# Kernel optimization log

Measured on AMD Instinct MI355X. Metric: run time of the kernel, lower is better.

Reference implementation:

```python
import jax, jax.numpy as jnp
import numpy as np

B, S = 32, 2048
D = 128      # embedding_dim
H = 256      # hidden_dim
K = 512      # codebook_size
RECON_COEF, COMMIT_COEF, VQ_COEF = 1.0, 0.15, 0.05


def _conv1d(x, w, b):
    # x: [B, Cin, S], w: [Cout, Cin, 3], 'SAME' padding (padding=1, k=3)
    y = jax.lax.conv_general_dilated(x, w, window_strides=(1,), padding='SAME',
                                     dimension_numbers=('NCH', 'OIH', 'NCH'))
    return y + b[None, :, None]


def _lrelu(x):
    return jnp.where(x >= 0, x, 0.2 * x)


def setup_inputs() -> dict:
    key = jax.random.key(0)
    ks = jax.random.split(key, 14)

    def w(k, shape, fan_in):
        bound = 1.0 / np.sqrt(fan_in)
        return jax.random.uniform(k, shape, jnp.float32, -bound, bound)

    return {
        'x': jax.random.normal(ks[0], (B, S), jnp.float32),
        'codebook': jax.random.normal(ks[1], (K, D), jnp.float32),
        'ew1': w(ks[2], (H, 1, 3), 1 * 3),  'eb1': w(ks[3], (H,), 1 * 3),
        'ew2': w(ks[4], (H, H, 3), H * 3),  'eb2': w(ks[5], (H,), H * 3),
        'ew3': w(ks[6], (D, H, 3), H * 3),  'eb3': w(ks[7], (D,), H * 3),
        'dw1': w(ks[8], (H, D, 3), D * 3),  'db1': w(ks[9], (H,), D * 3),
        'dw2': w(ks[10], (H, H, 3), H * 3), 'db2': w(ks[11], (H,), H * 3),
        'dw3': w(ks[12], (1, H, 3), H * 3), 'db3': w(ks[13], (1,), H * 3),
    }


def reference(x, codebook, ew1, eb1, ew2, eb2, ew3, eb3, dw1, db1, dw2, db2, dw3, db3):
    # ---- encode ----
    h = x[:, None, :]                                  # [B,1,S]
    h = _lrelu(_conv1d(h, ew1, eb1))
    h = _lrelu(_conv1d(h, ew2, eb2))
    z = _conv1d(h, ew3, eb3)                           # [B,D,S]

    # ---- vector quantize (eval mode: no EMA update) ----
    zt = jnp.transpose(z, (0, 2, 1))                   # [B,S,D]
    z_flat = zt.reshape(-1, D)                         # [B*S,D]
    # squared distances: |z|^2 + |c|^2 - 2 z c^T
    d = (jnp.sum(z_flat ** 2, axis=1, keepdims=True)
         + jnp.sum(codebook ** 2, axis=1)
         - 2.0 * z_flat @ codebook.T)                  # [B*S,K]
    idx = jnp.argmin(d, axis=1)                        # [B*S]
    z_q = codebook[idx].reshape(zt.shape)              # [B,S,D] (== one-hot @ codebook)

    vq_loss = jnp.mean((jax.lax.stop_gradient(zt) - z_q) ** 2) * VQ_COEF
    commitment_loss = jnp.mean((zt - jax.lax.stop_gradient(z_q)) ** 2) * COMMIT_COEF
    indices = idx.reshape(B, S)

    # ---- decode ----
    h = jnp.transpose(z_q, (0, 2, 1))                  # [B,D,S]
    h = _lrelu(_conv1d(h, dw1, db1))
    h = _lrelu(_conv1d(h, dw2, db2))
    x_recon = _conv1d(h, dw3, db3)[:, 0, :]            # [B,S]

    recon_loss = jnp.mean((x - x_recon) ** 2) * RECON_COEF
    loss = recon_loss + vq_loss + commitment_loss
    return x_recon, indices, loss, recon_loss, vq_loss, commitment_loss
```

## Files before the change

kernel.cpp:

```cpp
#include <hip/hip_runtime.h>
#include <float.h>

#define S_LEN 2048
#define BATCH 32
#define HCH   256
#define DCH   128
#define KCODES 512

typedef float  f32x4  __attribute__((ext_vector_type(4)));
typedef short  bf16x8 __attribute__((ext_vector_type(8)));
typedef short  short8 __attribute__((ext_vector_type(8)));

__device__ __forceinline__ float lrelu_f(float v) { return v >= 0.f ? v : 0.2f * v; }

__device__ __forceinline__ short f2bf(float f) {
    unsigned u = __float_as_uint(f);
    u = u + 0x7fffu + ((u >> 16) & 1u);
    return (short)(u >> 16);
}
__device__ __forceinline__ float bf2f(unsigned short u) {
    return __uint_as_float(((unsigned)u) << 16);
}

__device__ __forceinline__ void async_copy16(short* lds, const short* g) {
    __builtin_amdgcn_global_load_lds(
        (const __attribute__((address_space(1))) unsigned int*)g,
        (__attribute__((address_space(3))) unsigned int*)lds,
        16, 0, 0);
}

__global__ void prep_cb_split_kernel(const float* __restrict__ cb,
                                     short* __restrict__ cb_hi, short* __restrict__ cb_lo,
                                     float* __restrict__ cnorm) {
    int k = blockIdx.x * 256 + threadIdx.x;
    if (k < KCODES) {
        float s = 0.f;
        for (int d = 0; d < DCH; ++d) {
            float v = cb[k * DCH + d];
            s += v * v;
            short hi = f2bf(v);
            short lo = f2bf(v - bf2f((unsigned short)hi));
            cb_hi[k * DCH + d] = hi;
            cb_lo[k * DCH + d] = lo;
        }
        cnorm[k] = s;
    }
}

__global__ void prep_w_split_kernel(const float* __restrict__ Wsrc,
                                    short* __restrict__ Wh, short* __restrict__ Wl,
                                    int Cout, int Cin) {
    int i = blockIdx.x * 256 + threadIdx.x;
    int total = 3 * Cout * Cin;
    if (i < total) {
        int t = i / (Cout * Cin);
        int rem = i - t * Cout * Cin;
        int co = rem / Cin;
        int ci = rem - co * Cin;
        float v = Wsrc[(co * Cin + ci) * 3 + t];
        short hi = f2bf(v);
        Wh[i] = hi;
        Wl[i] = f2bf(v - bf2f((unsigned short)hi));
    }
}

__global__ void prep_wdec_kernel(const float* __restrict__ Wsrc, short* __restrict__ Wdst,
                                 int Cin) {
    int i = blockIdx.x * 256 + threadIdx.x;
    int total = 3 * 256 * Cin;
    if (i < total) {
        int t = i / (256 * Cin);
        int rem = i - t * 256 * Cin;
        int co = rem / Cin;
        int ci = rem - co * Cin;
        Wdst[i] = f2bf(Wsrc[(co * Cin + ci) * 3 + t]);
    }
}

__global__ void prep_w3t_kernel(const float* __restrict__ w3, float* __restrict__ w3t) {
    int i = blockIdx.x * 256 + threadIdx.x;
    if (i < 768) {
        int t = i / 256, ci = i - t * 256;
        w3t[i] = w3[ci * 3 + t];
    }
}

__global__ __launch_bounds__(256) void enc_conv1_cl_kernel(
        const float* __restrict__ x, short* __restrict__ h_hi, short* __restrict__ h_lo,
        const float* __restrict__ w, const float* __restrict__ bias) {
    __shared__ float ws[HCH * 3];
    __shared__ float bs[HCH];
    int tid = threadIdx.x;
    for (int i = tid; i < HCH * 3; i += 256) ws[i] = w[i];
    for (int i = tid; i < HCH; i += 256) bs[i] = bias[i];
    __syncthreads();
    int b = blockIdx.y;
    int s = blockIdx.x * 32 + (tid >> 3);
    int cch = tid & 7;
    const float* xb = x + (size_t)b * S_LEN;
    float xm = (s > 0) ? xb[s - 1] : 0.f;
    float x0 = xb[s];
    float xp = (s < S_LEN - 1) ? xb[s + 1] : 0.f;
    size_t base = ((size_t)(b * S_LEN + s)) * HCH + cch * 32;
#pragma unroll
    for (int cc = 0; cc < 4; ++cc) {
        short8 oh, ol;
#pragma unroll
        for (int e = 0; e < 8; ++e) {
            int co = cch * 32 + cc * 8 + e;
            float v = ws[co * 3 + 0] * xm + ws[co * 3 + 1] * x0 + ws[co * 3 + 2] * xp + bs[co];
            v = lrelu_f(v);
            short hi = f2bf(v);
            oh[e] = hi;
            ol[e] = f2bf(v - bf2f((unsigned short)hi));
        }
        *(short8*)(h_hi + base + cc * 8) = oh;
        *(short8*)(h_lo + base + cc * 8) = ol;
    }
}

__global__ __launch_bounds__(256, 3) void conv_mfma_split(
        const short* __restrict__ in_hi, const short* __restrict__ in_lo,
        short* __restrict__ out_hi, short* __restrict__ out_lo,
        const short* __restrict__ wt_hi, const short* __restrict__ wt_lo,
        const float* __restrict__ bias, int Cin, int Cout, int do_lrelu) {
    __shared__ short smem[16640];

    const int tid  = threadIdx.x;
    const int lane = tid & 63;
    const int w    = tid >> 6;
    const int m    = lane & 15;
    const int q    = lane >> 4;
    const int sOff = (w & 1) * 64;
    const int cOff = (w >> 1) * 64;
    const int b    = blockIdx.z;
    const int s0   = blockIdx.x * 128;
    const int co0  = blockIdx.y * 128;

    f32x4 acc[4][4];
    f32x4 zero4 = {0.f, 0.f, 0.f, 0.f};
#pragma unroll
    for (int i = 0; i < 4; ++i)
#pragma unroll
        for (int j = 0; j < 4; ++j) acc[i][j] = zero4;

    const short* inhb = in_hi + (size_t)b * S_LEN * Cin;
    const short* inlb = in_lo + (size_t)b * S_LEN * Cin;
    const char* XhB = (const char*)smem;
    const char* XlB = XhB + 1040 * 16;

    for (int ci0 = 0; ci0 < Cin; ci0 += 64) {
        __syncthreads();

        if (s0 == 0 && tid < 16) {
            short8 z = {0, 0, 0, 0, 0, 0, 0, 0};
            int buf = tid >> 3, slot = tid & 7;
            *(short8*)(smem + (size_t)(buf * 1040 + slot) * 8) = z;
        }
        if (s0 == S_LEN - 128 && tid < 16) {
            short8 z = {0, 0, 0, 0, 0, 0, 0, 0};
            int buf = tid >> 3, slot = tid & 7;
            *(short8*)(smem + (size_t)(buf * 1040 + 129 * 8 + slot) * 8) = z;
        }

        for (int c = tid; c < 2080; c += 256) {
            int base_c = c - lane;
            int buf  = (c >= 1040) ? 1 : 0;
            int cc   = c - buf * 1040;
            int r    = cc >> 3;
            int slot = cc & 7;
            int gch  = slot ^ (r & 7);
            int s    = s0 - 1 + r;
            short* ldsb = smem + (size_t)base_c * 8;
            const short* gp = (buf ? inlb : inhb) + (size_t)s * Cin + ci0 + gch * 8;
            if (s >= 0 && s < S_LEN) async_copy16(ldsb, gp);
        }
        __syncthreads();

#pragma unroll 1
        for (int ks = 0; ks < 2; ++ks) {
#pragma unroll
            for (int t = 0; t < 3; ++t) {
                bf16x8 ah[4], al[4], bh[4], bl[4];
#pragma unroll
                for (int i = 0; i < 4; ++i) {
                    int row = sOff + i * 16 + m + t;
                    int off = row * 128 + (((ks * 4 + q) ^ (row & 7)) << 4);
                    ah[i] = *(const bf16x8*)(XhB + off);
                    al[i] = *(const bf16x8*)(XlB + off);
                }
#pragma unroll
                for (int j = 0; j < 4; ++j) {
                    size_t woff = ((size_t)(t * Cout + co0 + cOff + j * 16 + m)) * Cin
                                  + ci0 + ks * 32 + q * 8;
                    bh[j] = *(const bf16x8*)(wt_hi + woff);
                    bl[j] = *(const bf16x8*)(wt_lo + woff);
                }
#pragma unroll
                for (int i = 0; i < 4; ++i)
#pragma unroll
                    for (int j = 0; j < 4; ++j) {
                        acc[i][j] = __builtin_amdgcn_mfma_f32_16x16x32_bf16(ah[i], bh[j], acc[i][j], 0, 0, 0);
                        acc[i][j] = __builtin_amdgcn_mfma_f32_16x16x32_bf16(ah[i], bl[j], acc[i][j], 0, 0, 0);
                        acc[i][j] = __builtin_amdgcn_mfma_f32_16x16x32_bf16(al[i], bh[j], acc[i][j], 0, 0, 0);
                    }
            }
        }
    }

    __syncthreads();

    short* ob = smem + w * 4096;
#pragma unroll
    for (int pass = 0; pass < 2; ++pass) {
#pragma unroll
        for (int j = 0; j < 4; ++j) {
            float bv = bias[co0 + cOff + j * 16 + m];
#pragma unroll
            for (int i = 0; i < 4; ++i)
#pragma unroll
                for (int r = 0; r < 4; ++r) {
                    float val = acc[i][j][r] + bv;
                    if (do_lrelu) val = lrelu_f(val);
                    short hi = f2bf(val);
                    short v = pass ? f2bf(val - bf2f((unsigned short)hi)) : hi;
                    ob[(i * 16 + q * 4 + r) * 64 + j * 16 + m] = v;
                }
        }
        short* outp = pass ? out_lo : out_hi;
#pragma unroll
        for (int itr = 0; itr < 8; ++itr) {
            int row = itr * 8 + (lane >> 3);
            int ch  = lane & 7;
            short8 v = *(const short8*)(ob + row * 64 + ch * 8);
            size_t goff = ((size_t)(b * S_LEN + s0 + sOff + row)) * Cout
                          + co0 + cOff + ch * 8;
            *(short8*)(outp + goff) = v;
        }
    }
}

__global__ __launch_bounds__(256) void vq_mfma_kernel(
        const short* __restrict__ z_hi, const short* __restrict__ z_lo,
        const short* __restrict__ cb_hi, const short* __restrict__ cb_lo,
        const float* __restrict__ cnorm, const float* __restrict__ cb,
        int* __restrict__ idx_out, float* __restrict__ idx_f_out,
        short* __restrict__ zq, float* __restrict__ acc_vq) {
    __shared__ short smem[2 * 64 * 136];
    __shared__ float redv[64][4];
    __shared__ int   redi[64][4];
    __shared__ int   idxs[64];
    __shared__ float wsum2[4];
    short* Zh = smem;
    short* Zl = smem + 64 * 136;

    const int tid = threadIdx.x;
    const int lane = tid & 63;
    const int w = tid >> 6;
    const int m = lane & 15;
    const int q = lane >> 4;
    const int n0 = blockIdx.x * 64;

    for (int c = tid; c < 2048; c += 256) {
        int buf = c >> 10;
        int rem = c & 1023;
        int r = rem >> 4, part = rem & 15;
        size_t goff = (size_t)(n0 + r) * DCH + part * 8;
        float4 v = buf ? *(const float4*)(z_lo + goff) : *(const float4*)(z_hi + goff);
        *(float4*)((buf ? Zl : Zh) + r * 136 + part * 8) = v;
    }
    __syncthreads();

    float best[4][4];
    int besti[4][4];
#pragma unroll
    for (int i = 0; i < 4; ++i)
#pragma unroll
        for (int r = 0; r < 4; ++r) { best[i][r] = FLT_MAX; besti[i][r] = 0; }

    for (int k0 = 0; k0 < KCODES; k0 += 256) {
        f32x4 acc[4][4];
        f32x4 zero4 = {0.f, 0.f, 0.f, 0.f};
#pragma unroll
        for (int i = 0; i < 4; ++i)
#pragma unroll
            for (int j = 0; j < 4; ++j) acc[i][j] = zero4;

#pragma unroll
        for (int d0 = 0; d0 < DCH; d0 += 32) {
            bf16x8 ah[4], al[4], bh[4], bl[4];
#pragma unroll
            for (int i = 0; i < 4; ++i) {
                int row = i * 16 + m;
                ah[i] = *(const bf16x8*)(Zh + row * 136 + d0 + q * 8);
                al[i] = *(const bf16x8*)(Zl + row * 136 + d0 + q * 8);
            }
#pragma unroll
            for (int j = 0; j < 4; ++j) {
                size_t coff = (size_t)(k0 + w * 64 + j * 16 + m) * DCH + d0 + q * 8;
                bh[j] = *(const bf16x8*)(cb_hi + coff);
                bl[j] = *(const bf16x8*)(cb_lo + coff);
            }
#pragma unroll
            for (int i = 0; i < 4; ++i)
#pragma unroll
                for (int j = 0; j < 4; ++j) {
                    acc[i][j] = __builtin_amdgcn_mfma_f32_16x16x32_bf16(ah[i], bh[j], acc[i][j], 0, 0, 0);
                    acc[i][j] = __builtin_amdgcn_mfma_f32_16x16x32_bf16(ah[i], bl[j], acc[i][j], 0, 0, 0);
                    acc[i][j] = __builtin_amdgcn_mfma_f32_16x16x32_bf16(al[i], bh[j], acc[i][j], 0, 0, 0);
                }
        }
#pragma unroll
        for (int j = 0; j < 4; ++j) {
            int k = k0 + w * 64 + j * 16 + m;
            float cn = cnorm[k];
#pragma unroll
            for (int i = 0; i < 4; ++i)
#pragma unroll
                for (int r = 0; r < 4; ++r) {
                    float dv = cn - 2.f * acc[i][j][r];
                    if (dv < best[i][r]) { best[i][r] = dv; besti[i][r] = k; }
                }
        }
    }

#pragma unroll
    for (int mask = 1; mask < 16; mask <<= 1) {
#pragma unroll
        for (int i = 0; i < 4; ++i)
#pragma unroll
            for (int r = 0; r < 4; ++r) {
                float ov = __shfl_xor(best[i][r], mask);
                int oi = __shfl_xor(besti[i][r], mask);
                if (ov < best[i][r] || (ov == best[i][r] && oi < besti[i][r])) {
                    best[i][r] = ov; besti[i][r] = oi;
                }
            }
    }
    if (m == 0) {
#pragma unroll
        for (int i = 0; i < 4; ++i)
#pragma unroll
            for (int r = 0; r < 4; ++r) {
                int srow = i * 16 + q * 4 + r;
                redv[srow][w] = best[i][r];
                redi[srow][w] = besti[i][r];
            }
    }
    __syncthreads();
    if (tid < 64) {
        float bv = redv[tid][0];
        int bi = redi[tid][0];
#pragma unroll
        for (int w2 = 1; w2 < 4; ++w2) {
            float v = redv[tid][w2];
            int ii = redi[tid][w2];
            if (v < bv || (v == bv && ii < bi)) { bv = v; bi = ii; }
        }
        int n = n0 + tid;
        idx_out[n] = bi;
        idx_f_out[n] = (float)bi;
        idxs[tid] = bi;
    }
    __syncthreads();

    {
        int r = tid >> 2;
        int dpart = tid & 3;
        int k = idxs[r];
        const float* src = cb + (size_t)k * DCH + dpart * 32;
        const short* zh = Zh + r * 136 + dpart * 32;
        const short* zl = Zl + r * 136 + dpart * 32;
        size_t zoff = (size_t)(n0 + r) * DCH + dpart * 32;
        float sum = 0.f;
#pragma unroll
        for (int h = 0; h < 4; ++h) {
            float4 f0 = *(const float4*)(src + h * 8);
            float4 f1 = *(const float4*)(src + h * 8 + 4);
            bf16x8 vh = *(const bf16x8*)(zh + h * 8);
            bf16x8 vl = *(const bf16x8*)(zl + h * 8);
            float qv[8] = {f0.x, f0.y, f0.z, f0.w, f1.x, f1.y, f1.z, f1.w};
            short8 o;
#pragma unroll
            for (int e = 0; e < 8; ++e) {
                o[e] = f2bf(qv[e]);
                float zv = bf2f((unsigned short)vh[e]) + bf2f((unsigned short)vl[e]);
                float df = zv - qv[e];
                sum += df * df;
            }
            *(short8*)(zq + zoff + h * 8) = o;
        }
        for (int off = 32; off > 0; off >>= 1) sum += __shfl_down(sum, off);
        if (lane == 0) wsum2[w] = sum;
    }
    __syncthreads();
    if (tid == 0) atomicAdd(acc_vq, wsum2[0] + wsum2[1] + wsum2[2] + wsum2[3]);
}

__global__ __launch_bounds__(256) void conv_mfma_cl(
        const short* __restrict__ in, short* __restrict__ out,
        const short* __restrict__ wt, const float* __restrict__ bias,
        int Cin) {
    __shared__ short smem[24672];
    short* Xs = smem;
    short* Ws = smem + 130 * 48;

    const int tid = threadIdx.x;
    const int lane = tid & 63;
    const int w = tid >> 6;
    const int m = lane & 15;
    const int q = lane >> 4;
    const int sOff = (w & 1) * 64;
    const int cOff = (w >> 1) * 64;
    const int b = blockIdx.z;
    const int s0 = blockIdx.x * 128;
    const int co0 = blockIdx.y * 128;

    f32x4 acc[4][4];
    f32x4 zero4 = {0.f, 0.f, 0.f, 0.f};
#pragma unroll
    for (int i = 0; i < 4; ++i)
#pragma unroll
        for (int j = 0; j < 4; ++j) acc[i][j] = zero4;

    const short* inb = in + (size_t)b * S_LEN * Cin;

    for (int ci0 = 0; ci0 < Cin; ci0 += 32) {
        __syncthreads();
        for (int c = tid; c < 520; c += 256) {
            int r = c >> 2, part = c & 3;
            int s = s0 - 1 + r;
            float4 v = make_float4(0.f, 0.f, 0.f, 0.f);
            if (s >= 0 && s < S_LEN)
                v = *(const float4*)(inb + (size_t)s * Cin + ci0 + part * 8);
            *(float4*)(Xs + r * 48 + part * 8) = v;
        }
        for (int c = tid; c < 1536; c += 256) {
            int t = c >> 9;
            int rem = c & 511;
            int cr = rem >> 2, part = rem & 3;
            float4 v = *(const float4*)(wt + ((size_t)(t * 256 + co0 + cr)) * Cin + ci0 + part * 8);
            *(float4*)(Ws + (t * 128 + cr) * 48 + part * 8) = v;
        }
        __syncthreads();

#pragma unroll
        for (int t = 0; t < 3; ++t) {
            bf16x8 a[4], bb[4];
#pragma unroll
            for (int i = 0; i < 4; ++i)
                a[i] = *(const bf16x8*)(Xs + (sOff + i * 16 + m + t) * 48 + q * 8);
#pragma unroll
            for (int j = 0; j < 4; ++j)
                bb[j] = *(const bf16x8*)(Ws + (t * 128 + cOff + j * 16 + m) * 48 + q * 8);
#pragma unroll
            for (int i = 0; i < 4; ++i)
#pragma unroll
                for (int j = 0; j < 4; ++j)
                    acc[i][j] = __builtin_amdgcn_mfma_f32_16x16x32_bf16(
                        a[i], bb[j], acc[i][j], 0, 0, 0);
        }
    }

    __syncthreads();

    short* ob = smem + w * (64 * 80);
#pragma unroll
    for (int j = 0; j < 4; ++j) {
        float bv = bias[co0 + cOff + j * 16 + m];
#pragma unroll
        for (int i = 0; i < 4; ++i) {
#pragma unroll
            for (int r = 0; r < 4; ++r) {
                float val = acc[i][j][r] + bv;
                val = lrelu_f(val);
                ob[(i * 16 + q * 4 + r) * 80 + j * 16 + m] = f2bf(val);
            }
        }
    }
    const int rsel = lane >> 3;
    const int off8 = (lane & 7) * 8;
#pragma unroll
    for (int pass = 0; pass < 8; ++pass) {
        int rr = pass * 8 + rsel;
        short8 v = *(const short8*)(ob + rr * 80 + off8);
        *(short8*)(out + ((size_t)(b * S_LEN + s0 + sOff + rr)) * 256 + co0 + cOff + off8) = v;
    }
}

__global__ __launch_bounds__(256) void dec_conv3_tiled_kernel(
        const short* __restrict__ h, const float* __restrict__ w3t,
        const float* __restrict__ b3, const float* __restrict__ x,
        float* __restrict__ xr, float* __restrict__ acc_recon) {
    __shared__ short Zs[66 * 264];
    __shared__ float ws[3 * 256];
    __shared__ float wsum[4];
    int tid = threadIdx.x;
    int b = blockIdx.y;
    int s0 = blockIdx.x * 64;
    const short* hb = h + (size_t)b * S_LEN * HCH;
    for (int i = tid; i < 768; i += 256) ws[i] = w3t[i];
    for (int c = tid; c < 2112; c += 256) {
        int r = c >> 5, part = c & 31;
        int g = s0 - 1 + r;
        short8 v = {0, 0, 0, 0, 0, 0, 0, 0};
        if (g >= 0 && g < S_LEN)
            v = *(const short8*)(hb + (size_t)g * HCH + part * 8);
        *(short8*)(Zs + r * 264 + part * 8) = v;
    }
    __syncthreads();

    int quarter = tid & 3;
    int sl = tid >> 2;
    float a0 = 0.f, a1 = 0.f, a2 = 0.f, a3 = 0.f;
#pragma unroll
    for (int t = 0; t < 3; ++t) {
        const short* zrow = Zs + (sl + t) * 264 + quarter * 64;
        const float* wrow = ws + t * 256 + quarter * 64;
#pragma unroll
        for (int c = 0; c < 8; ++c) {
            bf16x8 v = *(const bf16x8*)(zrow + c * 8);
            float4 w0 = *(const float4*)(wrow + c * 8);
            float4 w1 = *(const float4*)(wrow + c * 8 + 4);
            a0 = fmaf(w0.x, bf2f((unsigned short)v[0]), a0);
            a1 = fmaf(w0.y, bf2f((unsigned short)v[1]), a1);
            a2 = fmaf(w0.z, bf2f((unsigned short)v[2]), a2);
            a3 = fmaf(w0.w, bf2f((unsigned short)v[3]), a3);
            a0 = fmaf(w1.x, bf2f((unsigned short)v[4]), a0);
            a1 = fmaf(w1.y, bf2f((unsigned short)v[5]), a1);
            a2 = fmaf(w1.z, bf2f((unsigned short)v[6]), a2);
            a3 = fmaf(w1.w, bf2f((unsigned short)v[7]), a3);
        }
    }
    float acc = (a0 + a1) + (a2 + a3);
    acc += __shfl_xor(acc, 1);
    acc += __shfl_xor(acc, 2);
    float df2 = 0.f;
    if (quarter == 0) {
        int s = s0 + sl;
        float tot = acc + b3[0];
        xr[b * S_LEN + s] = tot;
        float df = x[b * S_LEN + s] - tot;
        df2 = df * df;
    }
    for (int off = 32; off > 0; off >>= 1) df2 += __shfl_down(df2, off);
    int lane = tid & 63, wv = tid >> 6;
    if (lane == 0) wsum[wv] = df2;
    __syncthreads();
    if (tid == 0) atomicAdd(acc_recon, wsum[0] + wsum[1] + wsum[2] + wsum[3]);
}

__global__ void finalize_kernel(const float* __restrict__ accs, float* __restrict__ out) {
    if (threadIdx.x == 0) {
        float vqm = accs[0] / ((float)BATCH * S_LEN * DCH);
        float rm  = accs[1] / ((float)BATCH * S_LEN);
        float vq_loss = vqm * 0.05f;
        float commit  = vqm * 0.15f;
        float recon   = rm * 1.0f;
        out[0] = recon + vq_loss + commit;
        out[1] = recon;
        out[2] = vq_loss;
        out[3] = commit;
    }
}

extern "C" void kernel_launch(void* const* d_in, const int* in_sizes, int n_in,
                              void* d_out, int out_size, void* d_ws, size_t ws_size,
                              hipStream_t stream) {
    const float* x    = (const float*)d_in[0];
    const float* cb   = (const float*)d_in[1];
    const float* ew1  = (const float*)d_in[2];
    const float* eb1  = (const float*)d_in[3];
    const float* ew2  = (const float*)d_in[4];
    const float* eb2  = (const float*)d_in[5];
    const float* ew3  = (const float*)d_in[6];
    const float* eb3  = (const float*)d_in[7];
    const float* dw1  = (const float*)d_in[8];
    const float* db1  = (const float*)d_in[9];
    const float* dw2  = (const float*)d_in[10];
    const float* db2  = (const float*)d_in[11];
    const float* dw3  = (const float*)d_in[12];
    const float* db3  = (const float*)d_in[13];

    float* out = (float*)d_out;
    float* xr    = out;
    float* idx_f = out + BATCH * S_LEN;
    float* loss_out = out + 2 * BATCH * S_LEN;

    const size_t NH = (size_t)BATCH * S_LEN * HCH;
    const size_t ND = (size_t)BATCH * S_LEN * DCH;

    short* sp = (short*)d_ws;
    short* h1_hi = sp;
    short* h1_lo = sp + NH;
    short* z_hi  = sp;
    short* z_lo  = sp + ND;
    short* h1d_bf = sp;
    short* h2_hi = sp + 2 * NH;
    short* h2_lo = sp + 3 * NH;
    short* zq_bf = sp + 2 * NH;
    short* h2d_bf = sp + 3 * NH;
    short* sm = sp + 4 * NH;
    short* cb_hi = sm; sm += KCODES * DCH;
    short* cb_lo = sm; sm += KCODES * DCH;
    short* w2_hi = sm; sm += 3 * HCH * HCH;
    short* w2_lo = sm; sm += 3 * HCH * HCH;
    short* w3_hi = sm; sm += 3 * DCH * HCH;
    short* w3_lo = sm; sm += 3 * DCH * HCH;
    short* wbf_d1 = sm; sm += 3 * 256 * DCH;
    short* wbf_d2 = sm; sm += 3 * 256 * HCH;
    float* cnorm = (float*)sm;
    int* idxb = (int*)(cnorm + KCODES);
    float* w3t = (float*)(idxb + BATCH * S_LEN);
    float* accs = w3t + 768;

    hipMemsetAsync(accs, 0, 2 * sizeof(float), stream);

    prep_cb_split_kernel<<<2, 256, 0, stream>>>(cb, cb_hi, cb_lo, cnorm);
    prep_w_split_kernel<<<(3 * HCH * HCH + 255) / 256, 256, 0, stream>>>(ew2, w2_hi, w2_lo, HCH, HCH);
    prep_w_split_kernel<<<(3 * DCH * HCH + 255) / 256, 256, 0, stream>>>(ew3, w3_hi, w3_lo, DCH, HCH);
    prep_wdec_kernel<<<(3 * 256 * DCH + 255) / 256, 256, 0, stream>>>(dw1, wbf_d1, DCH);
    prep_wdec_kernel<<<(3 * 256 * HCH + 255) / 256, 256, 0, stream>>>(dw2, wbf_d2, HCH);
    prep_w3t_kernel<<<3, 256, 0, stream>>>(dw3, w3t);

    enc_conv1_cl_kernel<<<dim3(S_LEN / 32, BATCH), 256, 0, stream>>>(x, h1_hi, h1_lo, ew1, eb1);
    conv_mfma_split<<<dim3(S_LEN / 128, HCH / 128, BATCH), 256, 0, stream>>>(
        h1_hi, h1_lo, h2_hi, h2_lo, w2_hi, w2_lo, eb2, HCH, HCH, 1);
    conv_mfma_split<<<dim3(S_LEN / 128, DCH / 128, BATCH), 256, 0, stream>>>(
        h2_hi, h2_lo, z_hi, z_lo, w3_hi, w3_lo, eb3, HCH, DCH, 0);

    vq_mfma_kernel<<<(BATCH * S_LEN) / 64, 256, 0, stream>>>(
        z_hi, z_lo, cb_hi, cb_lo, cnorm, cb, idxb, idx_f, zq_bf, accs);

    conv_mfma_cl<<<dim3(S_LEN / 128, 2, BATCH), 256, 0, stream>>>(
        zq_bf, h1d_bf, wbf_d1, db1, DCH);
    conv_mfma_cl<<<dim3(S_LEN / 128, 2, BATCH), 256, 0, stream>>>(
        h1d_bf, h2d_bf, wbf_d2, db2, HCH);
    dec_conv3_tiled_kernel<<<dim3(S_LEN / 64, BATCH), 256, 0, stream>>>(
        h2d_bf, w3t, db3, x, xr, accs + 1);

    finalize_kernel<<<1, 64, 0, stream>>>(accs, loss_out);
}
```

Before: 492.4 us.

## Restructure conv MFMA kernel with swizzled async LDS input and direct-global weights

The channels-last conv kernel now stages only the input tile in LDS, using async 16-byte copies into an XOR-swizzled layout to avoid bank conflicts. Weight fragments are read straight from global memory (relying on cache) rather than being staged in LDS. The input-channel step grows from 32 to 64, and launch bounds request 3 blocks per CU, which the smaller LDS footprint makes possible. The aim is fewer LDS stores and barriers and higher occupancy. The cost is more global/L2 traffic for weights and possible latency stalls before the MFMAs.

Measured after the change: 506.1 us. +2.8%, slower.

```diff
diff --git a/kernel.cpp b/kernel.cpp
--- a/kernel.cpp
+++ b/kernel.cpp
@@ -397,24 +397,22 @@
     if (tid == 0) atomicAdd(acc_vq, wsum2[0] + wsum2[1] + wsum2[2] + wsum2[3]);
 }
 
-__global__ __launch_bounds__(256) void conv_mfma_cl(
+__global__ __launch_bounds__(256, 3) void conv_mfma_cl(
         const short* __restrict__ in, short* __restrict__ out,
         const short* __restrict__ wt, const float* __restrict__ bias,
         int Cin) {
-    __shared__ short smem[24672];
-    short* Xs = smem;
-    short* Ws = smem + 130 * 48;
-
-    const int tid = threadIdx.x;
+    __shared__ short smem[16384];
+
+    const int tid  = threadIdx.x;
     const int lane = tid & 63;
-    const int w = tid >> 6;
-    const int m = lane & 15;
-    const int q = lane >> 4;
+    const int w    = tid >> 6;
+    const int m    = lane & 15;
+    const int q    = lane >> 4;
     const int sOff = (w & 1) * 64;
     const int cOff = (w >> 1) * 64;
-    const int b = blockIdx.z;
-    const int s0 = blockIdx.x * 128;
-    const int co0 = blockIdx.y * 128;
+    const int b    = blockIdx.z;
+    const int s0   = blockIdx.x * 128;
+    const int co0  = blockIdx.y * 128;
 
     f32x4 acc[4][4];
     f32x4 zero4 = {0.f, 0.f, 0.f, 0.f};
@@ -424,67 +422,82 @@
         for (int j = 0; j < 4; ++j) acc[i][j] = zero4;
 
     const short* inb = in + (size_t)b * S_LEN * Cin;
-
-    for (int ci0 = 0; ci0 < Cin; ci0 += 32) {
+    const char* XB = (const char*)smem;
+
+    for (int ci0 = 0; ci0 < Cin; ci0 += 64) {
         __syncthreads();
-        for (int c = tid; c < 520; c += 256) {
-            int r = c >> 2, part = c & 3;
-            int s = s0 - 1 + r;
-            float4 v = make_float4(0.f, 0.f, 0.f, 0.f);
-            if (s >= 0 && s < S_LEN)
-                v = *(const float4*)(inb + (size_t)s * Cin + ci0 + part * 8);
-            *(float4*)(Xs + r * 48 + part * 8) = v;
-        }
-        for (int c = tid; c < 1536; c += 256) {
-            int t = c >> 9;
-            int rem = c & 511;
-            int cr = rem >> 2, part = rem & 3;
-            float4 v = *(const float4*)(wt + ((size_t)(t * 256 + co0 + cr)) * Cin + ci0 + part * 8);
-            *(float4*)(Ws + (t * 128 + cr) * 48 + part * 8) = v;
+
+        if (s0 == 0 && tid < 8) {
+            short8 z = {0, 0, 0, 0, 0, 0, 0, 0};
+            *(short8*)(smem + (size_t)tid * 8) = z;
+        }
+        if (s0 == S_LEN - 128 && tid < 8) {
+            short8 z = {0, 0, 0, 0, 0, 0, 0, 0};
+            *(short8*)(smem + (size_t)(129 * 8 + tid) * 8) = z;
+        }
+
+        for (int c = tid; c < 1040; c += 256) {
+            int base_c = c - lane;
+            int r    = c >> 3;
+            int slot = c & 7;
+            int gch  = slot ^ (r & 7);
+            int s    = s0 - 1 + r;
+            short* ldsb = smem + (size_t)base_c * 8;
+            const short* gp = inb + (size_t)s * Cin + ci0 + gch * 8;
+            if (s >= 0 && s < S_LEN) async_copy16(ldsb, gp);
         }
         __syncthreads();
 
-#pragma unroll
-        for (int t = 0; t < 3; ++t) {
-            bf16x8 a[4], bb[4];
-#pragma unroll
-            for (int i = 0; i < 4; ++i)
-                a[i] = *(const bf16x8*)(Xs + (sOff + i * 16 + m + t) * 48 + q * 8);
-#pragma unroll
-            for (int j = 0; j < 4; ++j)
-                bb[j] = *(const bf16x8*)(Ws + (t * 128 + cOff + j * 16 + m) * 48 + q * 8);
-#pragma unroll
-            for (int i = 0; i < 4; ++i)
-#pragma unroll
-                for (int j = 0; j < 4; ++j)
-                    acc[i][j] = __builtin_amdgcn_mfma_f32_16x16x32_bf16(
-                        a[i], bb[j], acc[i][j], 0, 0, 0);
-        }
-    }
-
-    __syncthreads();
-
-    short* ob = smem + w * (64 * 80);
+#pragma unroll 1
+        for (int ks = 0; ks < 2; ++ks) {
+#pragma unroll
+            for (int t = 0; t < 3; ++t) {
+                bf16x8 a[4], bb[4];
+#pragma unroll
+                for (int i = 0; i < 4; ++i) {
+                    int row = sOff + i * 16 + m + t;
+                    int off = row * 128 + (((ks * 4 + q) ^ (row & 7)) << 4);
+                    a[i] = *(const bf16x8*)(XB + off);
+                }
+#pragma unroll
+                for (int j = 0; j < 4; ++j) {
+                    size_t woff = ((size_t)(t * 256 + co0 + cOff + j * 16 + m)) * Cin
+                                  + ci0 + ks * 32 + q * 8;
+                    bb[j] = *(const bf16x8*)(wt + woff);
+                }
+#pragma unroll
+                for (int i = 0; i < 4; ++i)
+#pragma unroll
+                    for (int j = 0; j < 4; ++j)
+                        acc[i][j] = __builtin_amdgcn_mfma_f32_16x16x32_bf16(
+                            a[i], bb[j], acc[i][j], 0, 0, 0);
+            }
+        }
+    }
+
+    __syncthreads();
+
+    short* ob = smem + w * 4096;
 #pragma unroll
     for (int j = 0; j < 4; ++j) {
         float bv = bias[co0 + cOff + j * 16 + m];
 #pragma unroll
-        for (int i = 0; i < 4; ++i) {
+        for (int i = 0; i < 4; ++i)
 #pragma unroll
             for (int r = 0; r < 4; ++r) {
                 float val = acc[i][j][r] + bv;
                 val = lrelu_f(val);
-                ob[(i * 16 + q * 4 + r) * 80 + j * 16 + m] = f2bf(val);
-            }
-        }
-    }
-    const int rsel = lane >> 3;
-    const int off8 = (lane & 7) * 8;
-#pragma unroll
-    for (int pass = 0; pass < 8; ++pass) {
-        int rr = pass * 8 + rsel;
-        short8 v = *(const short8*)(ob + rr * 80 + off8);
-        *(short8*)(out + ((size_t)(b * S_LEN + s0 + sOff + rr)) * 256 + co0 + cOff + off8) = v;
+                ob[(i * 16 + q * 4 + r) * 64 + j * 16 + m] = f2bf(val);
+            }
+    }
+#pragma unroll
+    for (int itr = 0; itr < 8; ++itr) {
+        int row = itr * 8 + (lane >> 3);
+        int ch  = lane & 7;
+        short8 v = *(const short8*)(ob + row * 64 + ch * 8);
+        size_t goff = ((size_t)(b * S_LEN + s0 + sOff + row)) * 256
+                      + co0 + cOff + ch * 8;
+        *(short8*)(out + goff) = v;
     }
 }
 
```

## Fuse final encoder conv with vector quantization and merge prep kernels

Applied to the files above, without the earlier changes.

The last encoder convolution now runs in the same kernel as the codebook search. Its hi/lo bf16 output goes straight into shared memory, so z no longer makes a round trip through global memory and one launch is dropped. The six weight and codebook preparation kernels are merged into one launch with a job index on the grid's y dimension. The cost is a larger, serialized fused kernel with launch bounds targeting two blocks per CU. The int index buffer is also removed.

Result: no change. 492.5 us (+0.0%).

```diff
diff --git a/kernel.cpp b/kernel.cpp
--- a/kernel.cpp
+++ b/kernel.cpp
@@ -29,59 +29,62 @@
         16, 0, 0);
 }
 
-__global__ void prep_cb_split_kernel(const float* __restrict__ cb,
-                                     short* __restrict__ cb_hi, short* __restrict__ cb_lo,
-                                     float* __restrict__ cnorm) {
-    int k = blockIdx.x * 256 + threadIdx.x;
-    if (k < KCODES) {
-        float s = 0.f;
-        for (int d = 0; d < DCH; ++d) {
-            float v = cb[k * DCH + d];
-            s += v * v;
+__global__ void prep_all_kernel(
+        const float* __restrict__ cb, short* __restrict__ cb_hi,
+        short* __restrict__ cb_lo, float* __restrict__ cnorm,
+        const float* __restrict__ ew2, short* __restrict__ w2_hi, short* __restrict__ w2_lo,
+        const float* __restrict__ ew3, short* __restrict__ w3_hi, short* __restrict__ w3_lo,
+        const float* __restrict__ dw1, short* __restrict__ wbf_d1,
+        const float* __restrict__ dw2, short* __restrict__ wbf_d2,
+        const float* __restrict__ dw3, float* __restrict__ w3t) {
+    const int job = blockIdx.y;
+    const int i = blockIdx.x * 256 + threadIdx.x;
+    if (job == 0) {
+        if (i < KCODES) {
+            float s = 0.f;
+            for (int d = 0; d < DCH; ++d) {
+                float v = cb[i * DCH + d];
+                s += v * v;
+                short hi = f2bf(v);
+                cb_hi[i * DCH + d] = hi;
+                cb_lo[i * DCH + d] = f2bf(v - bf2f((unsigned short)hi));
+            }
+            cnorm[i] = s;
+        }
+    } else if (job == 1 || job == 2) {
+        const int Cout = (job == 1) ? 256 : 128;
+        const int Cin = 256;
+        const float* src = (job == 1) ? ew2 : ew3;
+        short* Wh = (job == 1) ? w2_hi : w3_hi;
+        short* Wl = (job == 1) ? w2_lo : w3_lo;
+        int total = 3 * Cout * Cin;
+        if (i < total) {
+            int t = i / (Cout * Cin);
+            int rem = i - t * Cout * Cin;
+            int co = rem / Cin;
+            int ci = rem - co * Cin;
+            float v = src[(co * Cin + ci) * 3 + t];
             short hi = f2bf(v);
-            short lo = f2bf(v - bf2f((unsigned short)hi));
-            cb_hi[k * DCH + d] = hi;
-            cb_lo[k * DCH + d] = lo;
-        }
-        cnorm[k] = s;
-    }
-}
-
-__global__ void prep_w_split_kernel(const float* __restrict__ Wsrc,
-                                    short* __restrict__ Wh, short* __restrict__ Wl,
-                                    int Cout, int Cin) {
-    int i = blockIdx.x * 256 + threadIdx.x;
-    int total = 3 * Cout * Cin;
-    if (i < total) {
-        int t = i / (Cout * Cin);
-        int rem = i - t * Cout * Cin;
-        int co = rem / Cin;
-        int ci = rem - co * Cin;
-        float v = Wsrc[(co * Cin + ci) * 3 + t];
-        short hi = f2bf(v);
-        Wh[i] = hi;
-        Wl[i] = f2bf(v - bf2f((unsigned short)hi));
-    }
-}
-
-__global__ void prep_wdec_kernel(const float* __restrict__ Wsrc, short* __restrict__ Wdst,
-                                 int Cin) {
-    int i = blockIdx.x * 256 + threadIdx.x;
-    int total = 3 * 256 * Cin;
-    if (i < total) {
-        int t = i / (256 * Cin);
-        int rem = i - t * 256 * Cin;
-        int co = rem / Cin;
-        int ci = rem - co * Cin;
-        Wdst[i] = f2bf(Wsrc[(co * Cin + ci) * 3 + t]);
-    }
-}
-
-__global__ void prep_w3t_kernel(const float* __restrict__ w3, float* __restrict__ w3t) {
-    int i = blockIdx.x * 256 + threadIdx.x;
-    if (i < 768) {
-        int t = i / 256, ci = i - t * 256;
-        w3t[i] = w3[ci * 3 + t];
+            Wh[i] = hi;
+            Wl[i] = f2bf(v - bf2f((unsigned short)hi));
+        }
+    } else if (job == 3 || job == 4) {
+        const int Cin = (job == 3) ? 128 : 256;
+        const float* src = (job == 3) ? dw1 : dw2;
+        short* Wd = (job == 3) ? wbf_d1 : wbf_d2;
+        int total = 3 * 256 * Cin;
+        if (i < total) {
+            int t = i / (256 * Cin);
+            int rem = i - t * 256 * Cin;
+            int co = rem / Cin;
+            int ci = rem - co * Cin;
+            Wd[i] = f2bf(src[(co * Cin + ci) * 3 + t]);
+        }
+    } else {
+        if (i < 768) {
+            int t = i / 256, ci = i - t * 256;
+            w3t[i] = dw3[ci * 3 + t];
+        }
     }
 }
 
@@ -240,161 +243,253 @@
     }
 }
 
-__global__ __launch_bounds__(256) void vq_mfma_kernel(
-        const short* __restrict__ z_hi, const short* __restrict__ z_lo,
+__global__ __launch_bounds__(256, 2) void conv3_vq_kernel(
+        const short* __restrict__ in_hi, const short* __restrict__ in_lo,
+        const short* __restrict__ wt_hi, const short* __restrict__ wt_lo,
+        const float* __restrict__ bias,
         const short* __restrict__ cb_hi, const short* __restrict__ cb_lo,
         const float* __restrict__ cnorm, const float* __restrict__ cb,
-        int* __restrict__ idx_out, float* __restrict__ idx_f_out,
-        short* __restrict__ zq, float* __restrict__ acc_vq) {
-    __shared__ short smem[2 * 64 * 136];
+        float* __restrict__ idx_f_out, short* __restrict__ zq,
+        float* __restrict__ acc_vq) {
+    __shared__ short smem[17408];
     __shared__ float redv[64][4];
     __shared__ int   redi[64][4];
     __shared__ int   idxs[64];
     __shared__ float wsum2[4];
+
+    const int tid  = threadIdx.x;
+    const int lane = tid & 63;
+    const int w    = tid >> 6;
+    const int m    = lane & 15;
+    const int q    = lane >> 4;
+    const int sOff = (w & 1) * 64;
+    const int cOff = (w >> 1) * 64;
+    const int b    = blockIdx.y;
+    const int s0   = blockIdx.x * 128;
+    const int Cin  = HCH;
+
+    f32x4 acc[4][4];
+    f32x4 zero4 = {0.f, 0.f, 0.f, 0.f};
+#pragma unroll
+    for (int i = 0; i < 4; ++i)
+#pragma unroll
+        for (int j = 0; j < 4; ++j) acc[i][j] = zero4;
+
+    const short* inhb = in_hi + (size_t)b * S_LEN * Cin;
+    const short* inlb = in_lo + (size_t)b * S_LEN * Cin;
+    const char* XhB = (const char*)smem;
+    const char* XlB = XhB + 1040 * 16;
+
+    for (int ci0 = 0; ci0 < Cin; ci0 += 64) {
+        __syncthreads();
+
+        if (s0 == 0 && tid < 16) {
+            short8 z = {0, 0, 0, 0, 0, 0, 0, 0};
+            int buf = tid >> 3, slot = tid & 7;
+            *(short8*)(smem + (size_t)(buf * 1040 + slot) * 8) = z;
+        }
+        if (s0 == S_LEN - 128 && tid < 16) {
+            short8 z = {0, 0, 0, 0, 0, 0, 0, 0};
+            int buf = tid >> 3, slot = tid & 7;
+            *(short8*)(smem + (size_t)(buf * 1040 + 129 * 8 + slot) * 8) = z;
+        }
+
+        for (int c = tid; c < 2080; c += 256) {
+            int base_c = c - lane;
+            int buf  = (c >= 1040) ? 1 : 0;
+            int cc   = c - buf * 1040;
+            int r    = cc >> 3;
+            int slot = cc & 7;
+            int gch  = slot ^ (r & 7);
+            int s    = s0 - 1 + r;
+            short* ldsb = smem + (size_t)base_c * 8;
+            const short* gp = (buf ? inlb : inhb) + (size_t)s * Cin + ci0 + gch * 8;
+            if (s >= 0 && s < S_LEN) async_copy16(ldsb, gp);
+        }
+        __syncthreads();
+
+#pragma unroll 1
+        for (int ks = 0; ks < 2; ++ks) {
+#pragma unroll
+            for (int t = 0; t < 3; ++t) {
+                bf16x8 ah[4], al[4], bh[4], bl[4];
+#pragma unroll
+                for (int i = 0; i < 4; ++i) {
+                    int row = sOff + i * 16 + m + t;
+                    int off = row * 128 + (((ks * 4 + q) ^ (row & 7)) << 4);
+                    ah[i] = *(const bf16x8*)(XhB + off);
+                    al[i] = *(const bf16x8*)(XlB + off);
+                }
+#pragma unroll
+                for (int j = 0; j < 4; ++j) {
+                    size_t woff = ((size_t)(t * DCH + cOff + j * 16 + m)) * Cin
+                                  + ci0 + ks * 32 + q * 8;
+                    bh[j] = *(const bf16x8*)(wt_hi + woff);
+                    bl[j] = *(const bf16x8*)(wt_lo + woff);
+                }
+#pragma unroll
+                for (int i = 0; i < 4; ++i)
+#pragma unroll
+                    for (int j = 0; j < 4; ++j) {
+                        acc[i][j] = __builtin_amdgcn_mfma_f32_16x16x32_bf16(ah[i], bh[j], acc[i][j], 0, 0, 0);
+                        acc[i][j] = __builtin_amdgcn_mfma_f32_16x16x32_bf16(ah[i], bl[j], acc[i][j], 0, 0, 0);
+                        acc[i][j] = __builtin_amdgcn_mfma_f32_16x16x32_bf16(al[i], bh[j], acc[i][j], 0, 0, 0);
+                    }
+            }
+        }
+    }
+
+    __syncthreads();
+
     short* Zh = smem;
-    short* Zl = smem + 64 * 136;
-
-    const int tid = threadIdx.x;
-    const int lane = tid & 63;
-    const int w = tid >> 6;
-    const int m = lane & 15;
-    const int q = lane >> 4;
-    const int n0 = blockIdx.x * 64;
-
-    for (int c = tid; c < 2048; c += 256) {
-        int buf = c >> 10;
-        int rem = c & 1023;
-        int r = rem >> 4, part = rem & 15;
-        size_t goff = (size_t)(n0 + r) * DCH + part * 8;
-        float4 v = buf ? *(const float4*)(z_lo + goff) : *(const float4*)(z_hi + goff);
-        *(float4*)((buf ? Zl : Zh) + r * 136 + part * 8) = v;
-    }
-    __syncthreads();
-
-    float best[4][4];
-    int besti[4][4];
-#pragma unroll
-    for (int i = 0; i < 4; ++i)
-#pragma unroll
-        for (int r = 0; r < 4; ++r) { best[i][r] = FLT_MAX; besti[i][r] = 0; }
-
-    for (int k0 = 0; k0 < KCODES; k0 += 256) {
-        f32x4 acc[4][4];
-        f32x4 zero4 = {0.f, 0.f, 0.f, 0.f};
+    short* Zl = smem + 8704;
+
+#pragma unroll 1
+    for (int pass = 0; pass < 2; ++pass) {
+        if ((w & 1) == pass) {
+#pragma unroll
+            for (int j = 0; j < 4; ++j) {
+                float bv = bias[cOff + j * 16 + m];
+#pragma unroll
+                for (int i = 0; i < 4; ++i)
+#pragma unroll
+                    for (int r = 0; r < 4; ++r) {
+                        float val = acc[i][j][r] + bv;
+                        short hi = f2bf(val);
+                        short lo = f2bf(val - bf2f((unsigned short)hi));
+                        int rc = (i * 16 + q * 4 + r) * 136 + cOff + j * 16 + m;
+                        Zh[rc] = hi;
+                        Zl[rc] = lo;
+                    }
+            }
+        }
+        __syncthreads();
+
+        const int n0 = b * S_LEN + s0 + pass * 64;
+
+        float best[4][4];
+        int besti[4][4];
 #pragma unroll
         for (int i = 0; i < 4; ++i)
 #pragma unroll
-            for (int j = 0; j < 4; ++j) acc[i][j] = zero4;
-
-#pragma unroll
-        for (int d0 = 0; d0 < DCH; d0 += 32) {
-            bf16x8 ah[4], al[4], bh[4], bl[4];
-#pragma unroll
-            for (int i = 0; i < 4; ++i) {
-                int row = i * 16 + m;
-                ah[i] = *(const bf16x8*)(Zh + row * 136 + d0 + q * 8);
-                al[i] = *(const bf16x8*)(Zl + row * 136 + d0 + q * 8);
+            for (int r = 0; r < 4; ++r) { best[i][r] = FLT_MAX; besti[i][r] = 0; }
+
+#pragma unroll 1
+        for (int k0 = 0; k0 < KCODES; k0 += 256) {
+            f32x4 vacc[4][4];
+#pragma unroll
+            for (int i = 0; i < 4; ++i)
+#pragma unroll
+                for (int j = 0; j < 4; ++j) vacc[i][j] = zero4;
+
+#pragma unroll
+            for (int d0 = 0; d0 < DCH; d0 += 32) {
+                bf16x8 ah[4], al[4], bh[4], bl[4];
+#pragma unroll
+                for (int i = 0; i < 4; ++i) {
+                    int row = i * 16 + m;
+                    ah[i] = *(const bf16x8*)(Zh + row * 136 + d0 + q * 8);
+                    al[i] = *(const bf16x8*)(Zl + row * 136 + d0 + q * 8);
+                }
+#pragma unroll
+                for (int j = 0; j < 4; ++j) {
+                    size_t coff = (size_t)(k0 + w * 64 + j * 16 + m) * DCH + d0 + q * 8;
+                    bh[j] = *(const bf16x8*)(cb_hi + coff);
+                    bl[j] = *(const bf16x8*)(cb_lo + coff);
+                }
+#pragma unroll
+                for (int i = 0; i < 4; ++i)
+#pragma unroll
+                    for (int j = 0; j < 4; ++j) {
+                        vacc[i][j] = __builtin_amdgcn_mfma_f32_16x16x32_bf16(ah[i], bh[j], vacc[i][j], 0, 0, 0);
+                        vacc[i][j] = __builtin_amdgcn_mfma_f32_16x16x32_bf16(ah[i], bl[j], vacc[i][j], 0, 0, 0);
+                        vacc[i][j] = __builtin_amdgcn_mfma_f32_16x16x32_bf16(al[i], bh[j], vacc[i][j], 0, 0, 0);
+                    }
             }
 #pragma unroll
             for (int j = 0; j < 4; ++j) {
-                size_t coff = (size_t)(k0 + w * 64 + j * 16 + m) * DCH + d0 + q * 8;
-                bh[j] = *(const bf16x8*)(cb_hi + coff);
-                bl[j] = *(const bf16x8*)(cb_lo + coff);
-            }
+                int k = k0 + w * 64 + j * 16 + m;
+                float cn = cnorm[k];
+#pragma unroll
+                for (int i = 0; i < 4; ++i)
+#pragma unroll
+                    for (int r = 0; r < 4; ++r) {
+                        float dv = cn - 2.f * vacc[i][j][r];
+                        if (dv < best[i][r]) { best[i][r] = dv; besti[i][r] = k; }
+                    }
+            }
+        }
+
+#pragma unroll
+        for (int mask = 1; mask < 16; mask <<= 1) {
 #pragma unroll
             for (int i = 0; i < 4; ++i)
 #pragma unroll
-                for (int j = 0; j < 4; ++j) {
-                    acc[i][j] = __builtin_amdgcn_mfma_f32_16x16x32_bf16(ah[i], bh[j], acc[i][j], 0, 0, 0);
-                    acc[i][j] = __builtin_amdgcn_mfma_f32_16x16x32_bf16(ah[i], bl[j], acc[i][j], 0, 0, 0);
-                    acc[i][j] = __builtin_amdgcn_mfma_f32_16x16x32_bf16(al[i], bh[j], acc[i][j], 0, 0, 0);
-                }
-        }
-#pragma unroll
-        for (int j = 0; j < 4; ++j) {
-            int k = k0 + w * 64 + j * 16 + m;
-            float cn = cnorm[k];
+                for (int r = 0; r < 4; ++r) {
+                    float ov = __shfl_xor(best[i][r], mask);
+                    int oi = __shfl_xor(besti[i][r], mask);
+                    if (ov < best[i][r] || (ov == best[i][r] && oi < besti[i][r])) {
+                        best[i][r] = ov; besti[i][r] = oi;
+                    }
+                }
+        }
+        if (m == 0) {
 #pragma unroll
             for (int i = 0; i < 4; ++i)
 #pragma unroll
                 for (int r = 0; r < 4; ++r) {
-                    float dv = cn - 2.f * acc[i][j][r];
-                    if (dv < best[i][r]) { best[i][r] = dv; besti[i][r] = k; }
-                }
-        }
-    }
-
-#pragma unroll
-    for (int mask = 1; mask < 16; mask <<= 1) {
-#pragma unroll
-        for (int i = 0; i < 4; ++i)
-#pragma unroll
-            for (int r = 0; r < 4; ++r) {
-                float ov = __shfl_xor(best[i][r], mask);
-                int oi = __shfl_xor(besti[i][r], mask);
-                if (ov < best[i][r] || (ov == best[i][r] && oi < besti[i][r])) {
-                    best[i][r] = ov; besti[i][r] = oi;
-                }
-            }
-    }
-    if (m == 0) {
-#pragma unroll
-        for (int i = 0; i < 4; ++i)
-#pragma unroll
-            for (int r = 0; r < 4; ++r) {
-                int srow = i * 16 + q * 4 + r;
-                redv[srow][w] = best[i][r];
-                redi[srow][w] = besti[i][r];
-            }
-    }
-    __syncthreads();
-    if (tid < 64) {
-        float bv = redv[tid][0];
-        int bi = redi[tid][0];
-#pragma unroll
-        for (int w2 = 1; w2 < 4; ++w2) {
-            float v = redv[tid][w2];
-            int ii = redi[tid][w2];
-            if (v < bv || (v == bv && ii < bi)) { bv = v; bi = ii; }
-        }
-        int n = n0 + tid;
-        idx_out[n] = bi;
-        idx_f_out[n] = (float)bi;
-        idxs[tid] = bi;
-    }
-    __syncthreads();
-
-    {
-        int r = tid >> 2;
-        int dpart = tid & 3;
-        int k = idxs[r];
-        const float* src = cb + (size_t)k * DCH + dpart * 32;
-        const short* zh = Zh + r * 136 + dpart * 32;
-        const short* zl = Zl + r * 136 + dpart * 32;
-        size_t zoff = (size_t)(n0 + r) * DCH + dpart * 32;
-        float sum = 0.f;
-#pragma unroll
-        for (int h = 0; h < 4; ++h) {
-            float4 f0 = *(const float4*)(src + h * 8);
-            float4 f1 = *(const float4*)(src + h * 8 + 4);
-            bf16x8 vh = *(const bf16x8*)(zh + h * 8);
-            bf16x8 vl = *(const bf16x8*)(zl + h * 8);
-            float qv[8] = {f0.x, f0.y, f0.z, f0.w, f1.x, f1.y, f1.z, f1.w};
-            short8 o;
-#pragma unroll
-            for (int e = 0; e < 8; ++e) {
-                o[e] = f2bf(qv[e]);
-                float zv = bf2f((unsigned short)vh[e]) + bf2f((unsigned short)vl[e]);
-                float df = zv - qv[e];
-                sum += df * df;
-            }
-            *(short8*)(zq + zoff + h * 8) = o;
-        }
-        for (int off = 32; off > 0; off >>= 1) sum += __shfl_down(sum, off);
-        if (lane == 0) wsum2[w] = sum;
-    }
-    __syncthreads();
-    if (tid == 0) atomicAdd(acc_vq, wsum2[0] + wsum2[1] + wsum2[2] + wsum2[3]);
+                    int srow = i * 16 + q * 4 + r;
+                    redv[srow][w] = best[i][r];
+                    redi[srow][w] = besti[i][r];
+                }
+        }
+        __syncthreads();
+        if (tid < 64) {
+            float bv = redv[tid][0];
+            int bi = redi[tid][0];
+#pragma unroll
+            for (int w2 = 1; w2 < 4; ++w2) {
+                float v = redv[tid][w2];
+                int ii = redi[tid][w2];
+                if (v < bv || (v == bv && ii < bi)) { bv = v; bi = ii; }
+            }
+            idx_f_out[n0 + tid] = (float)bi;
+            idxs[tid] = bi;
+        }
+        __syncthreads();
+
+        {
+            int r = tid >> 2;
+            int dpart = tid & 3;
+            int k = idxs[r];
+            const float* src = cb + (size_t)k * DCH + dpart * 32;
+            const short* zh = Zh + r * 136 + dpart * 32;
+            const short* zl = Zl + r * 136 + dpart * 32;
+            size_t zoff = (size_t)(n0 + r) * DCH + dpart * 32;
+            float sum = 0.f;
+#pragma unroll
+            for (int h = 0; h < 4; ++h) {
+                float4 f0 = *(const float4*)(src + h * 8);
+                float4 f1 = *(const float4*)(src + h * 8 + 4);
+                bf16x8 vh = *(const bf16x8*)(zh + h * 8);
+                bf16x8 vl = *(const bf16x8*)(zl + h * 8);
+                float qv[8] = {f0.x, f0.y, f0.z, f0.w, f1.x, f1.y, f1.z, f1.w};
+                short8 o;
+#pragma unroll
+                for (int e = 0; e < 8; ++e) {
+                    o[e] = f2bf(qv[e]);
+                    float zv = bf2f((unsigned short)vh[e]) + bf2f((unsigned short)vl[e]);
+                    float df = zv - qv[e];
+                    sum += df * df;
+                }
+                *(short8*)(zq + zoff + h * 8) = o;
+            }
+            for (int off = 32; off > 0; off >>= 1) sum += __shfl_down(sum, off);
+            if (lane == 0) wsum2[w] = sum;
+        }
+        __syncthreads();
+        if (tid == 0) atomicAdd(acc_vq, wsum2[0] + wsum2[1] + wsum2[2] + wsum2[3]);
+    }
 }
 
 __global__ __launch_bounds__(256) void conv_mfma_cl(
@@ -593,12 +688,10 @@
     short* sp = (short*)d_ws;
     short* h1_hi = sp;
     short* h1_lo = sp + NH;
-    short* z_hi  = sp;
-    short* z_lo  = sp + ND;
-    short* h1d_bf = sp;
+    short* zq_bf = sp;
+    short* h1d_bf = sp + NH;
     short* h2_hi = sp + 2 * NH;
     short* h2_lo = sp + 3 * NH;
-    short* zq_bf = sp + 2 * NH;
     short* h2d_bf = sp + 3 * NH;
     short* sm = sp + 4 * NH;
     short* cb_hi = sm; sm += KCODES * DCH;
@@ -610,27 +703,22 @@
     short* wbf_d1 = sm; sm += 3 * 256 * DCH;
     short* wbf_d2 = sm; sm += 3 * 256 * HCH;
     float* cnorm = (float*)sm;
-    int* idxb = (int*)(cnorm + KCODES);
-    float* w3t = (float*)(idxb + BATCH * S_LEN);
+    float* w3t = cnorm + KCODES;
     float* accs = w3t + 768;
 
     hipMemsetAsync(accs, 0, 2 * sizeof(float), stream);
 
-    prep_cb_split_kernel<<<2, 256, 0, stream>>>(cb, cb_hi, cb_lo, cnorm);
-    prep_w_split_kernel<<<(3 * HCH * HCH + 255) / 256, 256, 0, stream>>>(ew2, w2_hi, w2_lo, HCH, HCH);
-    prep_w_split_kernel<<<(3 * DCH * HCH + 255) / 256, 256, 0, stream>>>(ew3, w3_hi, w3_lo, DCH, HCH);
-    prep_wdec_kernel<<<(3 * 256 * DCH + 255) / 256, 256, 0, stream>>>(dw1, wbf_d1, DCH);
-    prep_wdec_kernel<<<(3 * 256 * HCH + 255) / 256, 256, 0, stream>>>(dw2, wbf_d2, HCH);
-    prep_w3t_kernel<<<3, 256, 0, stream>>>(dw3, w3t);
+    prep_all_kernel<<<dim3(768, 6), 256, 0, stream>>>(
+        cb, cb_hi, cb_lo, cnorm, ew2, w2_hi, w2_lo, ew3, w3_hi, w3_lo,
+        dw1, wbf_d1, dw2, wbf_d2, dw3, w3t);
 
     enc_conv1_cl_kernel<<<dim3(S_LEN / 32, BATCH), 256, 0, stream>>>(x, h1_hi, h1_lo, ew1, eb1);
     conv_mfma_split<<<dim3(S_LEN / 128, HCH / 128, BATCH), 256, 0, stream>>>(
         h1_hi, h1_lo, h2_hi, h2_lo, w2_hi, w2_lo, eb2, HCH, HCH, 1);
-    conv_mfma_split<<<dim3(S_LEN / 128, DCH / 128, BATCH), 256, 0, stream>>>(
-        h2_hi, h2_lo, z_hi, z_lo, w3_hi, w3_lo, eb3, HCH, DCH, 0);
-
-    vq_mfma_kernel<<<(BATCH * S_LEN) / 64, 256, 0, stream>>>(
-        z_hi, z_lo, cb_hi, cb_lo, cnorm, cb, idxb, idx_f, zq_bf, accs);
+
+    conv3_vq_kernel<<<dim3(S_LEN / 128, BATCH), 256, 0, stream>>>(
+        h2_hi, h2_lo, w3_hi, w3_lo, eb3, cb_hi, cb_lo, cnorm, cb,
+        idx_f, zq_bf, accs);
 
     conv_mfma_cl<<<dim3(S_LEN / 128, 2, BATCH), 256, 0, stream>>>(
         zq_bf, h1d_bf, wbf_d1, db1, DCH);
```
